# Kernel optimization log

Measured on AMD Instinct MI355X. Metric: run time of the kernel, lower is better.

## Reference

```python
import jax, jax.numpy as jnp
import numpy as np


def setup_inputs() -> dict:
    key = jax.random.key(0)
    k1, k2, k3, k4 = jax.random.split(key, 4)
    B, N, D = 4, 2048, 1024
    scale = 1.0 / np.sqrt(D)
    return {
        "x": jax.random.normal(k1, (B, N, D), dtype=jnp.float32),
        "Wq": jax.random.normal(k2, (D, D), dtype=jnp.float32) * scale,
        "Wk": jax.random.normal(k3, (D, D), dtype=jnp.float32) * scale,
        "Wv": jax.random.normal(k4, (D, D), dtype=jnp.float32) * scale,
    }


def reference(x, Wq, Wk, Wv):
    # x: [b, n, d_in]; W*: [d_out, d_in] (torch Linear convention y = x @ W.T)
    q = jnp.einsum("bnd,od->bno", x, Wq)
    k = jnp.einsum("bnd,od->bno", x, Wk)
    v = jnp.einsum("bnd,od->bno", x, Wv)
    n = x.shape[1]
    d_out = k.shape[-1]
    scores = jnp.einsum("bqd,bkd->bqk", q, k)  # [b, n, n]
    causal = jnp.triu(jnp.ones((n, n), dtype=bool), k=1)  # True above diagonal
    scores = jnp.where(causal[None, :, :], -jnp.inf, scores)
    # NOTE: faithful to source -- softmax over dim=1 (query axis), not dim=-1
    attn = jax.nn.softmax(scores / jnp.sqrt(jnp.float32(d_out)), axis=1)
    # dropout p=0.0 (eval): identity
    return jnp.einsum("bqk,bkd->bqd", attn, v)
```

## Files before the change

kernel.cpp:

```cpp
#include <hip/hip_runtime.h>
#include <stdint.h>
#include <math.h>


typedef __attribute__((ext_vector_type(8))) short short8;
typedef __attribute__((ext_vector_type(4))) float f32x4;

static __device__ __forceinline__ ushort f2bf(float f) {
  union { float f; uint32_t u; } v; v.f = f;
  uint32_t r = v.u + 0x7FFFu + ((v.u >> 16) & 1u);
  return (ushort)(r >> 16);
}
static __device__ __forceinline__ float bf2f(ushort u) {
  union { uint32_t u; float f; } v; v.u = ((uint32_t)u) << 16;
  return v.f;
}

static __device__ __forceinline__ void gload_lds16(const ushort* g, ushort* l) {
  __builtin_amdgcn_global_load_lds(
      (const __attribute__((address_space(1))) void*)g,
      (__attribute__((address_space(3))) void*)l, 16, 0, 0);
}

#define SBAR()   __builtin_amdgcn_s_barrier()
#define SCHED0() __builtin_amdgcn_sched_barrier(0)
#define WAITL0() do { asm volatile("s_waitcnt lgkmcnt(0)" ::: "memory"); SCHED0(); } while (0)
#define WAITV4() asm volatile("s_waitcnt vmcnt(4)" ::: "memory")
#define WAITV3() asm volatile("s_waitcnt vmcnt(3)" ::: "memory")
#define WAITV0() asm volatile("s_waitcnt vmcnt(0)" ::: "memory")

__global__ void cast_all(const float* __restrict__ x, const float* __restrict__ Wv,
                         ushort* __restrict__ xb, ushort* __restrict__ Wvb,
                         int n_x4, int n_w4) {
  int i = blockIdx.x * blockDim.x + threadIdx.x;
  const float* src; ushort* dst; int off;
  if (i < n_x4) { src = x; dst = xb; off = i; }
  else { src = Wv; dst = Wvb; off = i - n_x4; }
  float4 v = ((const float4*)src)[off];
  ushort4 o;
  o.x = f2bf(v.x); o.y = f2bf(v.y); o.z = f2bf(v.z); o.w = f2bf(v.w);
  ((ushort4*)dst)[off] = o;
}

__global__ void cast_w_t(const float* __restrict__ Wq, const float* __restrict__ Wk,
                         ushort* __restrict__ WqT, ushort* __restrict__ WkT) {
  __shared__ ushort t[64][65];
  const float* src = blockIdx.z ? Wk : Wq;
  ushort* dst = blockIdx.z ? WkT : WqT;
  int c0 = blockIdx.x * 64, r0 = blockIdx.y * 64;
  int tid = threadIdx.x;
#pragma unroll
  for (int i = 0; i < 16; ++i) {
    int idx = i * 256 + tid, r = idx >> 6, c = idx & 63;
    t[r][c] = f2bf(src[(long)(r0 + r) * 1024 + c0 + c]);
  }
  __syncthreads();
#pragma unroll
  for (int i = 0; i < 16; ++i) {
    int idx = i * 256 + tid, r = idx >> 6, c = idx & 63;
    dst[(long)(c0 + r) * 1024 + r0 + c] = t[c][r];
  }
}

__global__ __launch_bounds__(256, 3) void gemm_g(
    const ushort* __restrict__ WkT, const ushort* __restrict__ WqT, ushort* __restrict__ Gt)
{
  const int D = 1024;
  const int bm0 = blockIdx.x * 128;
  const int bn0 = blockIdx.y * 128;
  const int nk = 32;

  __shared__ uint4 lds_v[49152 / 16];
  char* lds = (char*)lds_v;

  const int tid  = threadIdx.x;
  const int lane = tid & 63;
  const int wave = tid >> 6;
  const int wr   = wave >> 1;
  const int wc   = wave & 1;
  const int fr   = lane & 15;
  const int fg   = lane >> 4;

  f32x4 acc[4][4];
#pragma unroll
  for (int ii = 0; ii < 4; ++ii)
#pragma unroll
    for (int jj = 0; jj < 4; ++jj) acc[ii][jj] = (f32x4){0.f, 0.f, 0.f, 0.f};

  auto STAGE = [&](int tt) {
    if (tt >= nk) return;
    char* slab = lds + (tt % 3) * 16384;
#pragma unroll
    for (int u = 0; u < 2; ++u) {
      int s = u * 256 + tid;
      int row = s >> 2;
      int cc = (s & 3) ^ ((row >> 1) & 3);
      gload_lds16(WkT + (long)(bm0 + row) * D + tt * 32 + cc * 8,
                  (ushort*)(slab + s * 16));
    }
#pragma unroll
    for (int u = 0; u < 2; ++u) {
      int s = u * 256 + tid;
      int row = s >> 2;
      int cc = (s & 3) ^ ((row >> 1) & 3);
      gload_lds16(WqT + (long)(bn0 + row) * D + tt * 32 + cc * 8,
                  (ushort*)(slab + 8192 + s * 16));
    }
  };

  STAGE(0); STAGE(1);
  WAITV4();
  SBAR();

  for (int tt = 0; tt < nk; ++tt) {
    char* slab = lds + (tt % 3) * 16384;
    STAGE(tt + 2);
    short8 a[4], bf[4];
#pragma unroll
    for (int ii = 0; ii < 4; ++ii) {
      int row = wr * 64 + ii * 16 + fr;
      int cc = fg ^ ((row >> 1) & 3);
      a[ii] = *(const short8*)(slab + row * 64 + cc * 16);
    }
#pragma unroll
    for (int jj = 0; jj < 4; ++jj) {
      int row = wc * 64 + jj * 16 + fr;
      int cc = fg ^ ((row >> 1) & 3);
      bf[jj] = *(const short8*)(slab + 8192 + row * 64 + cc * 16);
    }
    WAITL0();
    __builtin_amdgcn_s_setprio(1);
#pragma unroll
    for (int ii = 0; ii < 4; ++ii)
#pragma unroll
      for (int jj = 0; jj < 4; ++jj)
        acc[ii][jj] = __builtin_amdgcn_mfma_f32_16x16x32_bf16(a[ii], bf[jj], acc[ii][jj], 0, 0, 0);
    __builtin_amdgcn_s_setprio(0);
    if (tt + 2 < nk) { WAITV4(); } else { WAITV0(); }
    SBAR();
  }

#pragma unroll
  for (int ii = 0; ii < 4; ++ii)
#pragma unroll
    for (int jj = 0; jj < 4; ++jj)
#pragma unroll
      for (int r = 0; r < 4; ++r) {
        int row = bm0 + wr * 64 + ii * 16 + fg * 4 + r;
        int col = bn0 + wc * 64 + jj * 16 + fr;
        Gt[(long)row * D + col] = f2bf(acc[ii][jj][r]);
      }
}

__global__ __launch_bounds__(512, 4) void proj_all(
    const ushort* __restrict__ xb, const ushort* __restrict__ Gt,
    const ushort* __restrict__ Wv, ushort* __restrict__ H, ushort* __restrict__ Vt)
{
  const int D = 1024;
  int L = blockIdx.x;
  L = (L & 7) * 64 + (L >> 3);

  const ushort* Ab; const ushort* Bb;
  int bm0, bn0;
  if (L < 256) {
    bm0 = (L >> 3) * 256;
    bn0 = (L & 7) * 128;
    Ab = xb;  Bb = Gt;
  } else {
    int rem = L - 256;
    bm0 = (rem >> 6) * 256;
    bn0 = (rem & 63) * 128;
    Ab = Wv;  Bb = xb;
  }

  const int nk = 32;

  __shared__ uint4 lds_v[73728 / 16];
  char* lds = (char*)lds_v;

  const int tid  = threadIdx.x;
  const int lane = tid & 63;
  const int wave = tid >> 6;
  const int wr   = wave >> 1;
  const int wc   = wave & 1;
  const int fr   = lane & 15;
  const int fg   = lane >> 4;

  f32x4 acc[4][4];
#pragma unroll
  for (int i = 0; i < 4; ++i)
#pragma unroll
    for (int j = 0; j < 4; ++j) acc[i][j] = (f32x4){0.f, 0.f, 0.f, 0.f};

  auto STAGE = [&](int tt) {
    if (tt >= nk) return;
    char* slab = lds + (tt % 3) * 24576;
#pragma unroll
    for (int u = 0; u < 2; ++u) {
      int s = u * 512 + tid;
      int row = s >> 2;
      int cc = (s & 3) ^ ((row >> 1) & 3);
      gload_lds16(Ab + (long)(bm0 + row) * D + tt * 32 + cc * 8,
                  (ushort*)(slab + s * 16));
    }
    {
      int s = tid;
      int row = s >> 2;
      int cc = (s & 3) ^ ((row >> 1) & 3);
      gload_lds16(Bb + (long)(bn0 + row) * D + tt * 32 + cc * 8,
                  (ushort*)(slab + 16384 + s * 16));
    }
  };

  STAGE(0); STAGE(1);
  WAITV3();
  SBAR();

  for (int t = 0; t < nk; ++t) {
    char* slab = lds + (t % 3) * 24576;
    STAGE(t + 2);

    short8 a[4], b[4];
#pragma unroll
    for (int i = 0; i < 4; ++i) {
      int row = wr * 64 + i * 16 + fr;
      int cc = fg ^ ((row >> 1) & 3);
      a[i] = *(const short8*)(slab + row * 64 + cc * 16);
    }
#pragma unroll
    for (int j = 0; j < 4; ++j) {
      int row = wc * 64 + j * 16 + fr;
      int cc = fg ^ ((row >> 1) & 3);
      b[j] = *(const short8*)(slab + 16384 + row * 64 + cc * 16);
    }
    WAITL0();
    __builtin_amdgcn_s_setprio(1);
#pragma unroll
    for (int i = 0; i < 4; ++i)
#pragma unroll
      for (int j = 0; j < 4; ++j)
        acc[i][j] = __builtin_amdgcn_mfma_f32_16x16x32_bf16(a[i], b[j], acc[i][j], 0, 0, 0);
    __builtin_amdgcn_s_setprio(0);

    if (t + 2 < nk) { WAITV3(); } else { WAITV0(); }
    SBAR();
  }

  if (L < 256) {
    ushort* Cb = H;
#pragma unroll
    for (int i = 0; i < 4; ++i)
#pragma unroll
      for (int j = 0; j < 4; ++j)
#pragma unroll
        for (int r = 0; r < 4; ++r) {
          int row = bm0 + wr * 64 + i * 16 + fg * 4 + r;
          int col = bn0 + wc * 64 + j * 16 + fr;
          Cb[(long)row * D + col] = f2bf(acc[i][j][r]);
        }
  } else {
    ushort* Cb = Vt + (long)(bn0 >> 11) * D * 2048;
#pragma unroll
    for (int i = 0; i < 4; ++i)
#pragma unroll
      for (int j = 0; j < 4; ++j)
#pragma unroll
        for (int r = 0; r < 4; ++r) {
          int row = bm0 + wr * 64 + i * 16 + fg * 4 + r;
          int col = (bn0 + wc * 64 + j * 16 + fr) & 2047;
          Cb[(long)row * 2048 + col] = f2bf(acc[i][j][r]);
        }
  }
}

__global__ __launch_bounds__(256, 3) void gemm_s(
    const ushort* __restrict__ Q, const ushort* __restrict__ Kb, ushort* __restrict__ S,
    float* __restrict__ pMg, float* __restrict__ pZg)
{
  const int NQ = 2048, D = 1024;
  int bid = blockIdx.x;
  bid = (bid & 7) * 68 + (bid >> 3);
  const int b = bid / 136;
  int t = bid - b * 136;
  int i = (int)((sqrtf(8.f * t + 1.f) - 1.f) * 0.5f);
  while ((i + 1) * (i + 2) / 2 <= t) ++i;
  while (i * (i + 1) / 2 > t) --i;
  const int j = t - i * (i + 1) / 2;
  const int bm0 = i * 128;
  const int bn0 = j * 128;

  const ushort* Ab = Q + (long)b * NQ * D;
  const ushort* Bb = Kb + (long)b * NQ * D;

  const int nk = 32;

  __shared__ uint4 lds_v[49152 / 16];
  char* lds = (char*)lds_v;

  const int tid  = threadIdx.x;
  const int lane = tid & 63;
  const int wave = tid >> 6;
  const int wr   = wave >> 1;
  const int wc   = wave & 1;
  const int fr   = lane & 15;
  const int fg   = lane >> 4;

  f32x4 acc[4][4];
#pragma unroll
  for (int ii = 0; ii < 4; ++ii)
#pragma unroll
    for (int jj = 0; jj < 4; ++jj) acc[ii][jj] = (f32x4){0.f, 0.f, 0.f, 0.f};

  auto STAGE = [&](int tt) {
    if (tt >= nk) return;
    char* slab = lds + (tt % 3) * 16384;
#pragma unroll
    for (int u = 0; u < 2; ++u) {
      int s = u * 256 + tid;
      int row = s >> 2;
      int cc = (s & 3) ^ ((row >> 1) & 3);
      gload_lds16(Ab + (long)(bm0 + row) * D + tt * 32 + cc * 8,
                  (ushort*)(slab + s * 16));
    }
#pragma unroll
    for (int u = 0; u < 2; ++u) {
      int s = u * 256 + tid;
      int row = s >> 2;
      int cc = (s & 3) ^ ((row >> 1) & 3);
      gload_lds16(Bb + (long)(bn0 + row) * D + tt * 32 + cc * 8,
                  (ushort*)(slab + 8192 + s * 16));
    }
  };

  STAGE(0); STAGE(1);
  WAITV4();
  SBAR();

  for (int tt = 0; tt < nk; ++tt) {
    char* slab = lds + (tt % 3) * 16384;
    STAGE(tt + 2);

    short8 a[4], bf[4];
#pragma unroll
    for (int ii = 0; ii < 4; ++ii) {
      int row = wr * 64 + ii * 16 + fr;
      int cc = fg ^ ((row >> 1) & 3);
      a[ii] = *(const short8*)(slab + row * 64 + cc * 16);
    }
#pragma unroll
    for (int jj = 0; jj < 4; ++jj) {
      int row = wc * 64 + jj * 16 + fr;
      int cc = fg ^ ((row >> 1) & 3);
      bf[jj] = *(const short8*)(slab + 8192 + row * 64 + cc * 16);
    }
    WAITL0();
    __builtin_amdgcn_s_setprio(1);
#pragma unroll
    for (int ii = 0; ii < 4; ++ii)
#pragma unroll
      for (int jj = 0; jj < 4; ++jj)
        acc[ii][jj] = __builtin_amdgcn_mfma_f32_16x16x32_bf16(a[ii], bf[jj], acc[ii][jj], 0, 0, 0);
    __builtin_amdgcn_s_setprio(0);

    if (tt + 2 < nk) { WAITV4(); } else { WAITV0(); }
    SBAR();
  }

  ushort* Cb = S + (long)b * NQ * NQ;
  float mcol[4];
#pragma unroll
  for (int jj = 0; jj < 4; ++jj) {
    const int colg = bn0 + wc * 64 + jj * 16 + fr;
    float m = -3.0e38f;
#pragma unroll
    for (int ii = 0; ii < 4; ++ii)
#pragma unroll
      for (int r = 0; r < 4; ++r) {
        int rowg = bm0 + wr * 64 + ii * 16 + fg * 4 + r;
        float v = acc[ii][jj][r] * 0.03125f;
        acc[ii][jj][r] = v;
        bool ok = rowg >= colg;
        Cb[(long)rowg * NQ + colg] = f2bf(ok ? __expf(v) : 0.f);
        m = ok ? fmaxf(m, v) : m;
      }
    m = fmaxf(m, __shfl_xor(m, 16));
    m = fmaxf(m, __shfl_xor(m, 32));
    mcol[jj] = m;
  }
  float* red = (float*)lds;
  if (fg == 0) {
#pragma unroll
    for (int jj = 0; jj < 4; ++jj)
      red[wr * 128 + wc * 64 + jj * 16 + fr] = mcol[jj];
  }
  SBAR();
  float Mf[4], zcol[4];
#pragma unroll
  for (int jj = 0; jj < 4; ++jj) {
    const int c = wc * 64 + jj * 16 + fr;
    Mf[jj] = fmaxf(red[c], red[128 + c]);
    const int colg = bn0 + c;
    float z = 0.f;
#pragma unroll
    for (int ii = 0; ii < 4; ++ii)
#pragma unroll
      for (int r = 0; r < 4; ++r) {
        int rowg = bm0 + wr * 64 + ii * 16 + fg * 4 + r;
        z += (rowg >= colg) ? __expf(acc[ii][jj][r] - Mf[jj]) : 0.f;
      }
    z += __shfl_xor(z, 16);
    z += __shfl_xor(z, 32);
    zcol[jj] = z;
  }
  if (fg == 0) {
#pragma unroll
    for (int jj = 0; jj < 4; ++jj)
      red[256 + wr * 128 + wc * 64 + jj * 16 + fr] = zcol[jj];
  }
  SBAR();
  if (wr == 0 && fg == 0) {
#pragma unroll
    for (int jj = 0; jj < 4; ++jj) {
      const int c = wc * 64 + jj * 16 + fr;
      long o = ((long)b * 16 + i) * NQ + bn0 + c;
      pMg[o] = Mf[jj];
      pZg[o] = red[256 + c] + red[256 + 128 + c];
    }
  }
}

__global__ void colstats_combine(const float* __restrict__ pM, const float* __restrict__ pZ,
                                 float* __restrict__ cvec, int Nq) {
  int idx = blockIdx.x * 256 + threadIdx.x;
  int b = idx / Nq, k = idx - b * Nq;
  const int i0 = k >> 7;
  const float* PM = pM + (long)b * 16 * Nq + k;
  const float* PZ = pZ + (long)b * 16 * Nq + k;
  float M = -3.0e38f;
  for (int c = i0; c < 16; ++c) M = fmaxf(M, PM[(long)c * Nq]);
  float Z = 0.f;
  for (int c = i0; c < 16; ++c) Z += PZ[(long)c * Nq] * __expf(PM[(long)c * Nq] - M);
  cvec[idx] = __expf(-M) / Z;
}

__global__ void scale_vt(ushort* __restrict__ Vt, const float* __restrict__ cvec,
                         int Nq, int Dd) {
  long t = (long)blockIdx.x * 256 + threadIdx.x;
  long nrow = t / (Nq / 8);
  int nb = (int)(t % (Nq / 8)) * 8;
  int b = (int)(nrow / Dd);
  ushort* p = Vt + nrow * Nq + nb;
  const float* c = cvec + (long)b * Nq + nb;
  union { uint4 v; ushort u[8]; } d, o;
  d.v = *(const uint4*)p;
#pragma unroll
  for (int j = 0; j < 8; ++j) o.u[j] = f2bf(bf2f(d.u[j]) * c[j]);
  *(uint4*)p = o.v;
}

__global__ __launch_bounds__(512, 4) void gemm_pv(
    const ushort* __restrict__ P, const ushort* __restrict__ Vt, float* __restrict__ out)
{
  const int NQ = 2048, DD = 1024;
  int L = blockIdx.x;
  L = (L & 7) * 64 + (L >> 3);
  const int pr = L & 7, dt = (L >> 3) & 15, b = L >> 7;

  const ushort* Pb = P + (long)b * NQ * NQ;
  const ushort* Vb = Vt + (long)b * DD * NQ + (long)(dt * 64) * NQ;
  float* Ob = out + (long)b * NQ * DD;

  __shared__ uint4 lds_v[73728 / 16];
  char* lds = (char*)lds_v;

  const int tid  = threadIdx.x;
  const int lane = tid & 63;
  const int wave = tid >> 6;
  const int wr   = wave >> 1;
  const int wc   = wave & 1;
  const int fr   = lane & 15;
  const int fg   = lane >> 4;

  for (int h = 0; h < 2; ++h) {
    const int tq = h ? (15 - pr) : pr;
    const int q0 = tq * 128;
    const ushort* Aq = Pb + (long)q0 * NQ;
    const int nk = (tq + 1) * 2;

    f32x4 acc[2][2];
#pragma unroll
    for (int i = 0; i < 2; ++i)
#pragma unroll
      for (int j = 0; j < 2; ++j) acc[i][j] = (f32x4){0.f, 0.f, 0.f, 0.f};

    auto STAGE = [&](int tt) {
      if (tt >= nk) return;
      char* slab = lds + (tt % 3) * 24576;
#pragma unroll
      for (int u = 0; u < 2; ++u) {
        int s = u * 512 + tid;
        int row = s >> 3;
        int cc = (s & 7) ^ (row & 7);
        gload_lds16(Aq + (long)row * NQ + tt * 64 + cc * 8,
                    (ushort*)(slab + s * 16));
      }
      {
        int s = tid;
        int row = s >> 3;
        int cc = (s & 7) ^ (row & 7);
        gload_lds16(Vb + (long)row * NQ + tt * 64 + cc * 8,
                    (ushort*)(slab + 16384 + s * 16));
      }
    };

    STAGE(0); STAGE(1);
    WAITV3();
    SBAR();

    for (int t = 0; t < nk; ++t) {
      char* slab = lds + (t % 3) * 24576;
      STAGE(t + 2);

#pragma unroll
      for (int kh = 0; kh < 2; ++kh) {
        short8 a[2], bfr[2];
#pragma unroll
        for (int i = 0; i < 2; ++i) {
          int row = wr * 32 + i * 16 + fr;
          int cc = (kh * 4 + fg) ^ (row & 7);
          a[i] = *(const short8*)(slab + row * 128 + cc * 16);
        }
#pragma unroll
        for (int j = 0; j < 2; ++j) {
          int row = wc * 32 + j * 16 + fr;
          int cc = (kh * 4 + fg) ^ (row & 7);
          bfr[j] = *(const short8*)(slab + 16384 + row * 128 + cc * 16);
        }
        WAITL0();
        __builtin_amdgcn_s_setprio(1);
#pragma unroll
        for (int i = 0; i < 2; ++i)
#pragma unroll
          for (int j = 0; j < 2; ++j)
            acc[i][j] = __builtin_amdgcn_mfma_f32_16x16x32_bf16(a[i], bfr[j], acc[i][j], 0, 0, 0);
        __builtin_amdgcn_s_setprio(0);
      }

      if (t + 2 < nk) { WAITV3(); } else { WAITV0(); }
      SBAR();
    }

#pragma unroll
    for (int i = 0; i < 2; ++i)
#pragma unroll
      for (int j = 0; j < 2; ++j)
#pragma unroll
        for (int r = 0; r < 4; ++r) {
          int row = q0 + wr * 32 + i * 16 + fg * 4 + r;
          int col = dt * 64 + wc * 32 + j * 16 + fr;
          Ob[(long)row * DD + col] = acc[i][j][r];
        }
  }
}

extern "C" void kernel_launch(void* const* d_in, const int* in_sizes, int n_in,
                              void* d_out, int out_size, void* d_ws, size_t ws_size,
                              hipStream_t stream) {
  const float* x  = (const float*)d_in[0];
  const float* Wq = (const float*)d_in[1];
  const float* Wk = (const float*)d_in[2];
  const float* Wv = (const float*)d_in[3];
  float* out = (float*)d_out;

  const int B = 4, N = 2048, D = 1024;
  const long BND = (long)B * N * D;

  char* ws = (char*)d_ws;
  ushort* xb  = (ushort*)ws;
  ushort* WqT = xb + BND;
  ushort* WkT = WqT + (long)D * D;
  ushort* Wvb = WkT + (long)D * D;
  ushort* Gt  = Wvb + (long)D * D;
  ushort* Hb  = Gt + (long)D * D;
  ushort* Vt  = Hb + BND;
  ushort* S   = Vt + BND;
  float*  pM  = (float*)(S + (long)B * N * N);
  float*  pZ  = pM + (long)B * 16 * N;
  float*  cv  = pZ + (long)B * 16 * N;

  {
    int n_x4 = (int)(BND / 4);
    int n_w4 = D * D / 4;
    cast_all<<<(n_x4 + n_w4) / 256, 256, 0, stream>>>(x, Wv, xb, Wvb, n_x4, n_w4);
  }
  {
    dim3 g(16, 16, 2);
    cast_w_t<<<g, 256, 0, stream>>>(Wq, Wk, WqT, WkT);
  }

  {
    dim3 g(8, 8);
    gemm_g<<<g, 256, 0, stream>>>(WkT, WqT, Gt);
  }

  proj_all<<<512, 512, 0, stream>>>(xb, Gt, Wvb, Hb, Vt);

  gemm_s<<<544, 256, 0, stream>>>(Hb, xb, S, pM, pZ);

  colstats_combine<<<(B * N) / 256, 256, 0, stream>>>(pM, pZ, cv, N);

  scale_vt<<<(int)(BND / 8 / 256), 256, 0, stream>>>(Vt, cv, N, D);

  gemm_pv<<<512, 512, 0, stream>>>(S, Vt, out);
}
```

Baseline: 149.5 us.

## Drop column-max stabilization in softmax and shrink gemm_g tiles to 64x64

The gemm_s epilogue no longer computes a per-column max. It writes exp(score) directly and accumulates the column sums in one pass, which removes a block barrier, the second exp pass and the pM buffer. colstats_combine now just sums the partial Z values and takes a reciprocal. Separately, gemm_g uses 64x64 tiles with a 16x16 grid to expose more blocks for the small 1024^3 weight GEMM. Skipping the max subtraction risks exp overflow or underflow for inputs with large scores, although the scores here are scaled by 1/32.

```diff
diff --git a/kernel.cpp b/kernel.cpp
--- a/kernel.cpp
+++ b/kernel.cpp
@@ -27,6 +27,7 @@
 #define WAITL0() do { asm volatile("s_waitcnt lgkmcnt(0)" ::: "memory"); SCHED0(); } while (0)
 #define WAITV4() asm volatile("s_waitcnt vmcnt(4)" ::: "memory")
 #define WAITV3() asm volatile("s_waitcnt vmcnt(3)" ::: "memory")
+#define WAITV2() asm volatile("s_waitcnt vmcnt(2)" ::: "memory")
 #define WAITV0() asm volatile("s_waitcnt vmcnt(0)" ::: "memory")
 
 __global__ void cast_all(const float* __restrict__ x, const float* __restrict__ Wv,
@@ -66,11 +67,11 @@
     const ushort* __restrict__ WkT, const ushort* __restrict__ WqT, ushort* __restrict__ Gt)
 {
   const int D = 1024;
-  const int bm0 = blockIdx.x * 128;
-  const int bn0 = blockIdx.y * 128;
+  const int bm0 = blockIdx.x * 64;
+  const int bn0 = blockIdx.y * 64;
   const int nk = 32;
 
-  __shared__ uint4 lds_v[49152 / 16];
+  __shared__ uint4 lds_v[24576 / 16];
   char* lds = (char*)lds_v;
 
   const int tid  = threadIdx.x;
@@ -81,73 +82,71 @@
   const int fr   = lane & 15;
   const int fg   = lane >> 4;
 
-  f32x4 acc[4][4];
-#pragma unroll
-  for (int ii = 0; ii < 4; ++ii)
-#pragma unroll
-    for (int jj = 0; jj < 4; ++jj) acc[ii][jj] = (f32x4){0.f, 0.f, 0.f, 0.f};
+  f32x4 acc[2][2];
+#pragma unroll
+  for (int ii = 0; ii < 2; ++ii)
+#pragma unroll
+    for (int jj = 0; jj < 2; ++jj) acc[ii][jj] = (f32x4){0.f, 0.f, 0.f, 0.f};
 
   auto STAGE = [&](int tt) {
     if (tt >= nk) return;
-    char* slab = lds + (tt % 3) * 16384;
-#pragma unroll
-    for (int u = 0; u < 2; ++u) {
-      int s = u * 256 + tid;
+    char* slab = lds + (tt % 3) * 8192;
+    {
+      int s = tid;
       int row = s >> 2;
       int cc = (s & 3) ^ ((row >> 1) & 3);
       gload_lds16(WkT + (long)(bm0 + row) * D + tt * 32 + cc * 8,
                   (ushort*)(slab + s * 16));
     }
-#pragma unroll
-    for (int u = 0; u < 2; ++u) {
-      int s = u * 256 + tid;
+    {
+      int s = tid;
       int row = s >> 2;
       int cc = (s & 3) ^ ((row >> 1) & 3);
       gload_lds16(WqT + (long)(bn0 + row) * D + tt * 32 + cc * 8,
-                  (ushort*)(slab + 8192 + s * 16));
+                  (ushort*)(slab + 4096 + s * 16));
     }
   };
 
   STAGE(0); STAGE(1);
-  WAITV4();
+  WAITV2();
   SBAR();
 
   for (int tt = 0; tt < nk; ++tt) {
-    char* slab = lds + (tt % 3) * 16384;
+    char* slab = lds + (tt % 3) * 8192;
     STAGE(tt + 2);
-    short8 a[4], bf[4];
-#pragma unroll
-    for (int ii = 0; ii < 4; ++ii) {
-      int row = wr * 64 + ii * 16 + fr;
+    short8 a[2], bf[2];
+#pragma unroll
+    for (int ii = 0; ii < 2; ++ii) {
+      int row = wr * 32 + ii * 16 + fr;
       int cc = fg ^ ((row >> 1) & 3);
       a[ii] = *(const short8*)(slab + row * 64 + cc * 16);
     }
 #pragma unroll
-    for (int jj = 0; jj < 4; ++jj) {
-      int row = wc * 64 + jj * 16 + fr;
+    for (int jj = 0; jj < 2; ++jj) {
+      int row = wc * 32 + jj * 16 + fr;
       int cc = fg ^ ((row >> 1) & 3);
-      bf[jj] = *(const short8*)(slab + 8192 + row * 64 + cc * 16);
+      bf[jj] = *(const short8*)(slab + 4096 + row * 64 + cc * 16);
     }
     WAITL0();
     __builtin_amdgcn_s_setprio(1);
 #pragma unroll
-    for (int ii = 0; ii < 4; ++ii)
-#pragma unroll
-      for (int jj = 0; jj < 4; ++jj)
+    for (int ii = 0; ii < 2; ++ii)
+#pragma unroll
+      for (int jj = 0; jj < 2; ++jj)
         acc[ii][jj] = __builtin_amdgcn_mfma_f32_16x16x32_bf16(a[ii], bf[jj], acc[ii][jj], 0, 0, 0);
     __builtin_amdgcn_s_setprio(0);
-    if (tt + 2 < nk) { WAITV4(); } else { WAITV0(); }
+    if (tt + 2 < nk) { WAITV2(); } else { WAITV0(); }
     SBAR();
   }
 
 #pragma unroll
-  for (int ii = 0; ii < 4; ++ii)
-#pragma unroll
-    for (int jj = 0; jj < 4; ++jj)
+  for (int ii = 0; ii < 2; ++ii)
+#pragma unroll
+    for (int jj = 0; jj < 2; ++jj)
 #pragma unroll
       for (int r = 0; r < 4; ++r) {
-        int row = bm0 + wr * 64 + ii * 16 + fg * 4 + r;
-        int col = bn0 + wc * 64 + jj * 16 + fr;
+        int row = bm0 + wr * 32 + ii * 16 + fg * 4 + r;
+        int col = bn0 + wc * 32 + jj * 16 + fr;
         Gt[(long)row * D + col] = f2bf(acc[ii][jj][r]);
       }
 }
@@ -275,7 +274,7 @@
 
 __global__ __launch_bounds__(256, 3) void gemm_s(
     const ushort* __restrict__ Q, const ushort* __restrict__ Kb, ushort* __restrict__ S,
-    float* __restrict__ pMg, float* __restrict__ pZg)
+    float* __restrict__ pZg)
 {
   const int NQ = 2048, D = 1024;
   int bid = blockIdx.x;
@@ -367,55 +366,30 @@
   }
 
   ushort* Cb = S + (long)b * NQ * NQ;
-  float mcol[4];
+  float zcol[4];
 #pragma unroll
   for (int jj = 0; jj < 4; ++jj) {
     const int colg = bn0 + wc * 64 + jj * 16 + fr;
-    float m = -3.0e38f;
+    float z = 0.f;
 #pragma unroll
     for (int ii = 0; ii < 4; ++ii)
 #pragma unroll
       for (int r = 0; r < 4; ++r) {
         int rowg = bm0 + wr * 64 + ii * 16 + fg * 4 + r;
-        float v = acc[ii][jj][r] * 0.03125f;
-        acc[ii][jj][r] = v;
         bool ok = rowg >= colg;
-        Cb[(long)rowg * NQ + colg] = f2bf(ok ? __expf(v) : 0.f);
-        m = ok ? fmaxf(m, v) : m;
-      }
-    m = fmaxf(m, __shfl_xor(m, 16));
-    m = fmaxf(m, __shfl_xor(m, 32));
-    mcol[jj] = m;
-  }
-  float* red = (float*)lds;
-  if (fg == 0) {
-#pragma unroll
-    for (int jj = 0; jj < 4; ++jj)
-      red[wr * 128 + wc * 64 + jj * 16 + fr] = mcol[jj];
-  }
-  SBAR();
-  float Mf[4], zcol[4];
-#pragma unroll
-  for (int jj = 0; jj < 4; ++jj) {
-    const int c = wc * 64 + jj * 16 + fr;
-    Mf[jj] = fmaxf(red[c], red[128 + c]);
-    const int colg = bn0 + c;
-    float z = 0.f;
-#pragma unroll
-    for (int ii = 0; ii < 4; ++ii)
-#pragma unroll
-      for (int r = 0; r < 4; ++r) {
-        int rowg = bm0 + wr * 64 + ii * 16 + fg * 4 + r;
-        z += (rowg >= colg) ? __expf(acc[ii][jj][r] - Mf[jj]) : 0.f;
+        float e = ok ? __expf(acc[ii][jj][r] * 0.03125f) : 0.f;
+        Cb[(long)rowg * NQ + colg] = f2bf(e);
+        z += e;
       }
     z += __shfl_xor(z, 16);
     z += __shfl_xor(z, 32);
     zcol[jj] = z;
   }
+  float* red = (float*)lds;
   if (fg == 0) {
 #pragma unroll
     for (int jj = 0; jj < 4; ++jj)
-      red[256 + wr * 128 + wc * 64 + jj * 16 + fr] = zcol[jj];
+      red[wr * 128 + wc * 64 + jj * 16 + fr] = zcol[jj];
   }
   SBAR();
   if (wr == 0 && fg == 0) {
@@ -423,24 +397,20 @@
     for (int jj = 0; jj < 4; ++jj) {
       const int c = wc * 64 + jj * 16 + fr;
       long o = ((long)b * 16 + i) * NQ + bn0 + c;
-      pMg[o] = Mf[jj];
-      pZg[o] = red[256 + c] + red[256 + 128 + c];
-    }
-  }
-}
-
-__global__ void colstats_combine(const float* __restrict__ pM, const float* __restrict__ pZ,
-                                 float* __restrict__ cvec, int Nq) {
+      pZg[o] = red[c] + red[128 + c];
+    }
+  }
+}
+
+__global__ void colstats_combine(const float* __restrict__ pZ, float* __restrict__ cvec,
+                                 int Nq) {
   int idx = blockIdx.x * 256 + threadIdx.x;
   int b = idx / Nq, k = idx - b * Nq;
   const int i0 = k >> 7;
-  const float* PM = pM + (long)b * 16 * Nq + k;
   const float* PZ = pZ + (long)b * 16 * Nq + k;
-  float M = -3.0e38f;
-  for (int c = i0; c < 16; ++c) M = fmaxf(M, PM[(long)c * Nq]);
   float Z = 0.f;
-  for (int c = i0; c < 16; ++c) Z += PZ[(long)c * Nq] * __expf(PM[(long)c * Nq] - M);
-  cvec[idx] = __expf(-M) / Z;
+  for (int c = i0; c < 16; ++c) Z += PZ[(long)c * Nq];
+  cvec[idx] = 1.0f / Z;
 }
 
 __global__ void scale_vt(ushort* __restrict__ Vt, const float* __restrict__ cvec,
@@ -584,8 +554,7 @@
   ushort* Hb  = Gt + (long)D * D;
   ushort* Vt  = Hb + BND;
   ushort* S   = Vt + BND;
-  float*  pM  = (float*)(S + (long)B * N * N);
-  float*  pZ  = pM + (long)B * 16 * N;
+  float*  pZ  = (float*)(S + (long)B * N * N);
   float*  cv  = pZ + (long)B * 16 * N;
 
   {
@@ -599,15 +568,15 @@
   }
 
   {
-    dim3 g(8, 8);
+    dim3 g(16, 16);
     gemm_g<<<g, 256, 0, stream>>>(WkT, WqT, Gt);
   }
 
   proj_all<<<512, 512, 0, stream>>>(xb, Gt, Wvb, Hb, Vt);
 
-  gemm_s<<<544, 256, 0, stream>>>(Hb, xb, S, pM, pZ);
-
-  colstats_combine<<<(B * N) / 256, 256, 0, stream>>>(pM, pZ, cv, N);
+  gemm_s<<<544, 256, 0, stream>>>(Hb, xb, S, pZ);
+
+  colstats_combine<<<(B * N) / 256, 256, 0, stream>>>(pZ, cv, N);
 
   scale_vt<<<(int)(BND / 8 / 256), 256, 0, stream>>>(Vt, cv, N, D);
 
```

New measurement: 139.3 us. -6.8%, faster.
